# Kernel tuning notes

Measured on AMD Instinct MI355X. Metric: run time of the kernel, lower is better.

## Reference

```python
import jax, jax.numpy as jnp
import numpy as np

V, C, S, H, B, T = 10000, 1024, 128, 256, 16, 128
NEG = -1e10


def _mlp(x, w1, b1, w2, b2, wo, bo):
    # ResidualLayer (dropout=0, eval): relu(lin1) -> relu(lin2 + residual), then final Linear
    h = jax.nn.relu(x @ w1 + b1)
    h = jax.nn.relu(h @ w2 + b2 + x)
    return h @ wo + bo


def setup_inputs() -> dict:
    key = jax.random.key(0)
    ks = iter(jax.random.split(key, 32))
    d = {}
    d["text"] = jax.random.randint(next(ks), (B, T), 0, V)
    d["word2state"] = jax.random.randint(next(ks), (V, S), 0, C)

    def rn(shape, scale):
        return jax.random.normal(next(ks), shape, dtype=jnp.float32) * scale

    s = 1.0 / np.sqrt(H)
    d["start_emb"] = rn((C, H), 1.0)
    d["start_w1"], d["start_b1"] = rn((H, H), s), jnp.zeros((H,), jnp.float32)
    d["start_w2"], d["start_b2"] = rn((H, H), s), jnp.zeros((H,), jnp.float32)
    d["start_wo"], d["start_bo"] = rn((H, 1), s), jnp.zeros((1,), jnp.float32)
    d["state_emb"] = rn((C, H), 1.0)
    d["trans_w1"], d["trans_b1"] = rn((H, H), s), jnp.zeros((H,), jnp.float32)
    d["trans_w2"], d["trans_b2"] = rn((H, H), s), jnp.zeros((H,), jnp.float32)
    d["trans_wo"], d["trans_bo"] = rn((H, C), s), jnp.zeros((C,), jnp.float32)
    d["pre_emb"] = rn((C, H), 1.0)
    d["term_w1"], d["term_b1"] = rn((H, H), s), jnp.zeros((H,), jnp.float32)
    d["term_w2"], d["term_b2"] = rn((H, H), s), jnp.zeros((H,), jnp.float32)
    d["term_wo"], d["term_bo"] = rn((H, V), s), jnp.zeros((V,), jnp.float32)
    return d


def _evidence(text, word2state,
              start_emb, start_w1, start_b1, start_w2, start_b2, start_wo, start_bo,
              state_emb, trans_w1, trans_b1, trans_w2, trans_b2, trans_wo, trans_bo,
              pre_emb, term_w1, term_b1, term_w2, term_b2, term_wo, term_bo):
    # start distribution over C states
    start = jax.nn.log_softmax(
        _mlp(start_emb, start_w1, start_b1, start_w2, start_b2, start_wo, start_bo)[:, 0])
    # transition [C, C]
    transition = jax.nn.log_softmax(
        _mlp(state_emb, trans_w1, trans_b1, trans_w2, trans_b2, trans_wo, trans_bo), axis=-1)
    # emission with sparse state->word mask (scatter of word2state)
    em_logits = _mlp(pre_emb, term_w1, term_b1, term_w2, term_b2, term_wo, term_bo)  # [C, V]
    a = jnp.repeat(jnp.arange(V), S)  # word index per (word, slot)
    mask = jnp.zeros((C, V), dtype=bool).at[word2state.reshape(-1), a].set(True)
    emission = jax.nn.log_softmax(jnp.where(mask, em_logits, NEG), axis=-1)  # [C, V]

    clamped = word2state[text]  # [B, T, S] states allowed per token
    init = start[clamped[:, 0]]  # [B, S]
    # transition restricted to clamped states: [B, T-1, S_prev, S_next]
    lp = transition[clamped[:, :-1, :, None], clamped[:, 1:, None, :]]
    obs = emission[clamped, text[:, :, None]]  # [B, T, S]
    lp = lp + obs[:, 1:, None, :]                     # emission of next token
    lp = lp.at[:, 0].add(init[:, :, None] + obs[:, 0, :, None])
    lp = jnp.swapaxes(lp, -1, -2)  # [B, T-1, S_next, S_prev]

    # forward algorithm (log-space scan)
    alpha = jax.nn.logsumexp(lp[:, 0], axis=-1)  # [B, S]
    pots = jnp.swapaxes(lp[:, 1:], 0, 1)  # [T-2, B, S, S]

    def step(a_prev, pot):
        return jax.nn.logsumexp(pot + a_prev[:, None, :], axis=-1), None

    alpha_T, _ = jax.lax.scan(step, alpha, pots)
    return jax.nn.logsumexp(alpha_T, axis=-1).sum()


def reference(text, word2state,
              start_emb, start_w1, start_b1, start_w2, start_b2, start_wo, start_bo,
              state_emb, trans_w1, trans_b1, trans_w2, trans_b2, trans_wo, trans_bo,
              pre_emb, term_w1, term_b1, term_w2, term_b2, term_wo, term_bo):
    return _evidence(text, word2state,
                     start_emb, start_w1, start_b1, start_w2, start_b2, start_wo, start_bo,
                     state_emb, trans_w1, trans_b1, trans_w2, trans_b2, trans_wo, trans_bo,
                     pre_emb, term_w1, term_b1, term_w2, term_b2, term_wo, term_bo)
```

## Files before the change

### kernel.cpp

```cpp
#include <hip/hip_runtime.h>
#include <hip/hip_bf16.h>

#define V 10000
#define VP 10112
#define C 1024
#define S 128
#define H 256
#define B 16
#define T 128
#define NR 64
#define CHUNK 158
#define NRP 158
#define LDK 40
#define SPITCH 1032

#define TIX(r,g) (((r)<<7) + ((((g) ^ ((r)&7)))<<3))

typedef unsigned short u16;
typedef unsigned int u32;
typedef __bf16 bf16x8 __attribute__((ext_vector_type(8)));
typedef float f32x4 __attribute__((ext_vector_type(4)));

static __device__ __forceinline__ float bf2f(u16 x){ return __uint_as_float(((u32)x)<<16); }
static __device__ __forceinline__ u16 f2bf(float f){ u32 u=__float_as_uint(f); return (u16)((u + 0x7FFFu + ((u>>16)&1u))>>16); }

struct Cvt3 { const float* s0; const float* s1; const float* s2; u16* d0; u16* d1; u16* d2; };
__global__ __launch_bounds__(256) void k_cvt3(Cvt3 a){
  const float* s = (blockIdx.y==0)? a.s0 : (blockIdx.y==1)? a.s1 : a.s2;
  u16* d = (blockIdx.y==0)? a.d0 : (blockIdx.y==1)? a.d1 : a.d2;
  int i = (blockIdx.x*256 + threadIdx.x)*8;
  float4 x0 = *(const float4*)(s+i);
  float4 x1 = *(const float4*)(s+i+4);
  u16 h[8] = {f2bf(x0.x),f2bf(x0.y),f2bf(x0.z),f2bf(x0.w),f2bf(x1.x),f2bf(x1.y),f2bf(x1.z),f2bf(x1.w)};
  *(uint4*)(d+i) = *(uint4*)h;
}

__global__ __launch_bounds__(256) void k_transpose(const float* __restrict__ src, u16* __restrict__ dst, int N){
  __shared__ float tile[32][33];
  int v0 = blockIdx.x*32, k0 = blockIdx.y*32;
  int tx = threadIdx.x, ty = threadIdx.y;
  for (int i=0;i<32;i+=8){
    int k = k0+ty+i, v = v0+tx;
    tile[ty+i][tx] = (v < N) ? src[(size_t)k*N + v] : 0.f;
  }
  __syncthreads();
  for (int i=0;i<32;i+=8){
    int v = v0+ty+i, k = k0+tx;
    dst[(size_t)v*H + k] = f2bf(tile[tx][ty+i]);
  }
}

struct T6 { const float* s[6]; u16* d[6]; };
__global__ __launch_bounds__(256) void k_transpose6(T6 a){
  const float* src = a.s[blockIdx.z];
  u16* dst = a.d[blockIdx.z];
  __shared__ float tile[32][33];
  int v0 = blockIdx.x*32, k0 = blockIdx.y*32;
  int tx = threadIdx.x, ty = threadIdx.y;
  for (int i=0;i<32;i+=8){
    int k = k0+ty+i, v = v0+tx;
    tile[ty+i][tx] = src[(size_t)k*H + v];
  }
  __syncthreads();
  for (int i=0;i<32;i+=8){
    int v = v0+ty+i, k = k0+tx;
    dst[(size_t)v*H + k] = f2bf(tile[tx][ty+i]);
  }
}

struct M3 { const u16* A[3]; const u16* W[3]; const float* bias[3]; const u16* R[3]; u16* O[3]; };
template<int RESID>
__global__ __launch_bounds__(256) void k_mlpg(M3 a){
  const int z = blockIdx.z;
  const u16* A  = a.A[z];
  const u16* BT = a.W[z];
  const float* bias = a.bias[z];
  const u16* Rm = a.R[z];
  u16* O = a.O[z];
  __shared__ u16 As[128*LDK];
  __shared__ u16 Bs[128*LDK];
  const int tid = threadIdx.x;
  const int lane = tid & 63, wave = tid >> 6;
  const int wm = wave >> 1, wn = wave & 1;
  const int m0 = blockIdx.y * 128, n0 = blockIdx.x * 128;
  const int lr = lane & 15, lg = lane >> 4;
  f32x4 acc[4][4] = {};
  const int sr = tid >> 1, sh = (tid & 1) * 16;
  for (int ks = 0; ks < H; ks += 32){
    const u16* ga = A  + (size_t)(m0 + sr)*H + ks + sh;
    const u16* gb = BT + (size_t)(n0 + sr)*H + ks + sh;
    uint4 a0 = *(const uint4*)ga;
    uint4 a1 = *(const uint4*)(ga + 8);
    uint4 b0 = *(const uint4*)gb;
    uint4 b1 = *(const uint4*)(gb + 8);
    __syncthreads();
    *(uint4*)&As[sr*LDK + sh]     = a0;
    *(uint4*)&As[sr*LDK + sh + 8] = a1;
    *(uint4*)&Bs[sr*LDK + sh]     = b0;
    *(uint4*)&Bs[sr*LDK + sh + 8] = b1;
    __syncthreads();
    bf16x8 af[4], bfr[4];
    #pragma unroll
    for (int m=0;m<4;m++) af[m]  = *(const bf16x8*)&As[(wm*64 + m*16 + lr)*LDK + lg*8];
    #pragma unroll
    for (int n=0;n<4;n++) bfr[n] = *(const bf16x8*)&Bs[(wn*64 + n*16 + lr)*LDK + lg*8];
    #pragma unroll
    for (int m=0;m<4;m++)
      #pragma unroll
      for (int n=0;n<4;n++)
        acc[m][n] = __builtin_amdgcn_mfma_f32_16x16x32_bf16(af[m], bfr[n], acc[m][n], 0,0,0);
  }
  #pragma unroll
  for (int m=0;m<4;m++){
    int r_g = m0 + wm*64 + m*16 + lg*4;
    #pragma unroll
    for (int n=0;n<4;n++){
      int n_g = n0 + wn*64 + n*16 + lr;
      float bv = bias[n_g];
      #pragma unroll
      for (int reg=0; reg<4; reg++){
        int r = r_g + reg;
        float val = acc[m][n][reg] + bv;
        if (RESID) val += bf2f(Rm[(size_t)r*H + n_g]);
        val = fmaxf(val, 0.f);
        O[(size_t)r*H + n_g] = f2bf(val);
      }
    }
  }
}

__global__ __launch_bounds__(1024) void k_start(
    const u16* __restrict__ h2, const float* __restrict__ wo, const float* __restrict__ bo,
    float* __restrict__ start_lp){
  const int c = threadIdx.x;
  const int lane = c & 63, wid = c >> 6;
  __shared__ float red[16];
  __shared__ float Ms, Zs;
  float acc = bo[0];
  const u16* row = h2 + (size_t)c*H;
  for (int k=0;k<H;k+=8){
    uint4 hv = *(const uint4*)(row+k);
    float4 w0 = *(const float4*)(wo+k);
    float4 w1 = *(const float4*)(wo+k+4);
    acc = fmaf(bf2f((u16)(hv.x&0xFFFFu)), w0.x, acc);
    acc = fmaf(bf2f((u16)(hv.x>>16)),     w0.y, acc);
    acc = fmaf(bf2f((u16)(hv.y&0xFFFFu)), w0.z, acc);
    acc = fmaf(bf2f((u16)(hv.y>>16)),     w0.w, acc);
    acc = fmaf(bf2f((u16)(hv.z&0xFFFFu)), w1.x, acc);
    acc = fmaf(bf2f((u16)(hv.z>>16)),     w1.y, acc);
    acc = fmaf(bf2f((u16)(hv.w&0xFFFFu)), w1.z, acc);
    acc = fmaf(bf2f((u16)(hv.w>>16)),     w1.w, acc);
  }
  float m = acc;
  for (int o=1;o<64;o<<=1) m = fmaxf(m, __shfl_xor(m,o));
  if (lane==0) red[wid]=m;
  __syncthreads();
  if (c==0){ float t=red[0]; for(int i=1;i<16;i++) t=fmaxf(t,red[i]); Ms=t; }
  __syncthreads();
  float M = Ms;
  float e = expf(acc - M);
  float sum = e;
  for (int o=1;o<64;o<<=1) sum += __shfl_xor(sum,o);
  __syncthreads();
  if (lane==0) red[wid]=sum;
  __syncthreads();
  if (c==0){ float t=0.f; for(int i=0;i<16;i++) t+=red[i]; Zs=t; }
  __syncthreads();
  start_lp[c] = acc - (M + logf(Zs));
}

template<int BIAS_ROW, int BF16OUT, int COLMAX>
__global__ __launch_bounds__(256) void k_gemm(
    const u16* __restrict__ A, const u16* __restrict__ BT,
    const float* __restrict__ bias, int biasBound,
    void* __restrict__ outp, int ldout, float* __restrict__ cmax){
  __shared__ u16 As[128*LDK];
  __shared__ u16 Bs[128*LDK];
  const int tid = threadIdx.x;
  const int lane = tid & 63, wave = tid >> 6;
  const int wm = wave >> 1, wn = wave & 1;
  const int m0 = blockIdx.y * 128, n0 = blockIdx.x * 128;
  const int lr = lane & 15, lg = lane >> 4;
  f32x4 acc[4][4] = {};
  const int sr = tid >> 1, sh = (tid & 1) * 16;
  for (int ks = 0; ks < H; ks += 32){
    const u16* ga = A  + (size_t)(m0 + sr)*H + ks + sh;
    const u16* gb = BT + (size_t)(n0 + sr)*H + ks + sh;
    uint4 a0 = *(const uint4*)ga;
    uint4 a1 = *(const uint4*)(ga + 8);
    uint4 b0 = *(const uint4*)gb;
    uint4 b1 = *(const uint4*)(gb + 8);
    __syncthreads();
    *(uint4*)&As[sr*LDK + sh]     = a0;
    *(uint4*)&As[sr*LDK + sh + 8] = a1;
    *(uint4*)&Bs[sr*LDK + sh]     = b0;
    *(uint4*)&Bs[sr*LDK + sh + 8] = b1;
    __syncthreads();
    bf16x8 af[4], bfr[4];
    #pragma unroll
    for (int m=0;m<4;m++) af[m]  = *(const bf16x8*)&As[(wm*64 + m*16 + lr)*LDK + lg*8];
    #pragma unroll
    for (int n=0;n<4;n++) bfr[n] = *(const bf16x8*)&Bs[(wn*64 + n*16 + lr)*LDK + lg*8];
    #pragma unroll
    for (int m=0;m<4;m++)
      #pragma unroll
      for (int n=0;n<4;n++)
        acc[m][n] = __builtin_amdgcn_mfma_f32_16x16x32_bf16(af[m], bfr[n], acc[m][n], 0,0,0);
  }
  float cmx[4] = {-1e30f,-1e30f,-1e30f,-1e30f};
  #pragma unroll
  for (int m=0;m<4;m++){
    int r_g = m0 + wm*64 + m*16 + lg*4;
    #pragma unroll
    for (int n=0;n<4;n++){
      int n_g = n0 + wn*64 + n*16 + lr;
      float bcol = BIAS_ROW ? 0.f : bias[n_g];
      #pragma unroll
      for (int reg=0; reg<4; reg++){
        int r = r_g + reg;
        float bv = BIAS_ROW ? ((r < biasBound) ? bias[r] : 0.f) : bcol;
        float val = acc[m][n][reg] + bv;
        if (COLMAX) cmx[n] = fmaxf(cmx[n], val);
        if (BF16OUT) ((u16*)outp)[(size_t)r*ldout + n_g] = f2bf(val);
        else         ((float*)outp)[(size_t)r*ldout + n_g] = val;
      }
    }
  }
  if (COLMAX){
    #pragma unroll
    for (int n=0;n<4;n++){
      float m_ = cmx[n];
      m_ = fmaxf(m_, __shfl_xor(m_,16));
      m_ = fmaxf(m_, __shfl_xor(m_,32));
      if (lg==0) cmax[((size_t)(blockIdx.y*2 + wm))*C + n0 + wn*64 + n*16 + lr] = m_;
    }
  }
}

__global__ __launch_bounds__(256) void k_softmax(const float* __restrict__ TL, u16* __restrict__ P){
  const int c = blockIdx.x;
  const int tid = threadIdx.x, lane = tid & 63, wid = tid >> 6;
  __shared__ float red[4];
  __shared__ float Ms, Zs;
  float4 v = ((const float4*)(TL + (size_t)c*C))[tid];
  float m = fmaxf(fmaxf(v.x,v.y), fmaxf(v.z,v.w));
  for (int o=1;o<64;o<<=1) m = fmaxf(m, __shfl_xor(m,o));
  if (lane==0) red[wid] = m;
  __syncthreads();
  if (tid==0) Ms = fmaxf(fmaxf(red[0],red[1]), fmaxf(red[2],red[3]));
  __syncthreads();
  float M = Ms;
  float e0 = expf(v.x-M), e1 = expf(v.y-M), e2 = expf(v.z-M), e3 = expf(v.w-M);
  float s = (e0+e1)+(e2+e3);
  for (int o=1;o<64;o<<=1) s += __shfl_xor(s,o);
  if (lane==0) red[wid] = s;
  __syncthreads();
  if (tid==0) Zs = red[0]+red[1]+red[2]+red[3];
  __syncthreads();
  float inv = 1.f/Zs;
  u32 lo = (u32)f2bf(e0*inv) | ((u32)f2bf(e1*inv)<<16);
  u32 hi = (u32)f2bf(e2*inv) | ((u32)f2bf(e3*inv)<<16);
  *(uint2*)(P + (size_t)c*C + tid*4) = make_uint2(lo, hi);
}

__global__ void k_shiftc(const float* __restrict__ shiftp, float* __restrict__ shift){
  int c = threadIdx.x + blockIdx.x*blockDim.x;
  if (c < C){
    float m = -1e30f;
    for (int r=0;r<NRP;r++) m = fmaxf(m, shiftp[(size_t)r*C + c]);
    shift[c] = m;
  }
}

__global__ __launch_bounds__(256) void k_scatter(
    const int* __restrict__ w2s, const u16* __restrict__ EM,
    const float* __restrict__ shift, u16* __restrict__ D){
  int idx = blockIdx.x*256 + threadIdx.x;
  int v = idx >> 7;
  const int c = w2s[idx];
  float val = bf2f(EM[(size_t)v*C + c]);
  D[(size_t)v*C + c] = f2bf(expf(val - shift[c]));
}

__global__ __launch_bounds__(256) void k_colsum(const u16* __restrict__ D, float* __restrict__ sumexp){
  const int c = blockIdx.x*256 + threadIdx.x;
  const int v0 = blockIdx.y*CHUNK;
  float s = 0.f;
  const u16* p = D + (size_t)v0*C + c;
  #pragma unroll 2
  for (int i=0;i<CHUNK;i++){ s += bf2f(p[0]); p += C; }
  sumexp[(size_t)blockIdx.y*C + c] = s;
}

__global__ void k_lse(const float* __restrict__ shift, const float* __restrict__ sumexp, float* __restrict__ lse){
  int c = threadIdx.x + blockIdx.x*blockDim.x;
  if (c < C){
    float s = 0.f;
    for (int r=0;r<NR;r++) s += sumexp[(size_t)r*C + c];
    lse[c] = shift[c] + logf(s);
  }
}

__global__ __launch_bounds__(128) void k_obs(
    const int* __restrict__ text, const int* __restrict__ w2s,
    const u16* __restrict__ EM, const float* __restrict__ lse,
    float* __restrict__ obs){
  const int bt = blockIdx.x;
  const int s = threadIdx.x;
  const int v = text[bt];
  const int c = w2s[(size_t)v*S + s];
  obs[(size_t)bt*S + s] = bf2f(EM[(size_t)v*C + c]) - lse[c];
}

__global__ __launch_bounds__(256) void k_pair0(
    const int* __restrict__ text, const int* __restrict__ w2s,
    const float* __restrict__ start_lp, const float* __restrict__ obs,
    const u16* __restrict__ P, u16* __restrict__ out, float* __restrict__ scales){
  const int j = blockIdx.x;
  const int b = blockIdx.y;
  const int t0 = 2*j, t1 = 2*j+1;
  __shared__ __align__(16) u16 tile[128*128];
  __shared__ __align__(16) u16 stage[8*SPITCH];
  __shared__ int cp0[S], cp1[S], cn1[S];
  __shared__ float eo0[S], eo1[S], a00[S];
  __shared__ float red[4];
  const int tid = threadIdx.x;
  if (tid < 128){
    int s = tid;
    int cpv = w2s[(size_t)text[b*T + t0]*S + s];
    cp0[s] = cpv;
    cp1[s] = w2s[(size_t)text[b*T + t0+1]*S + s];
    eo0[s] = expf(obs[((size_t)b*T + t0 + 1)*S + s]);
    a00[s] = (t0==0) ? expf(start_lp[cpv] + obs[(size_t)(b*T)*S + s]) : 1.0f;
  } else if (t1 < 127){
    int s = tid-128;
    cn1[s] = w2s[(size_t)text[b*T + t1+1]*S + s];
    eo1[s] = expf(obs[((size_t)b*T + t1 + 1)*S + s]);
  }
  __syncthreads();
  const int lane = tid & 63, wave = tid >> 6;
  const int wm = wave >> 1, wn = wave & 1;
  const int lr = lane & 15, lg = lane >> 4;
  for (int c8 = 0; c8 < 16; ++c8){
    #pragma unroll
    for (int p=0;p<4;p++){
      int idx = p*256 + tid;
      int r = idx >> 7, col16 = idx & 127;
      *(uint4*)&stage[r*SPITCH + col16*8] = *(const uint4*)&P[(size_t)cp0[c8*8 + r]*C + col16*8];
    }
    __syncthreads();
    {
      int r = tid >> 5, kh = tid & 31;
      float asp = a00[c8*8 + r];
      u16 h4[4];
      #pragma unroll
      for (int q=0;q<4;q++){
        int k = kh*4 + q;
        h4[q] = f2bf(bf2f(stage[r*SPITCH + cp1[k]]) * eo0[k] * asp);
      }
      *(uint2*)&tile[TIX(c8*8 + r, kh>>1) + (kh&1)*4] = *(uint2*)h4;
    }
    __syncthreads();
  }
  bf16x8 bfr[4][4];
  #pragma unroll
  for (int n=0;n<4;n++)
    #pragma unroll
    for (int kc=0;kc<4;kc++)
      bfr[n][kc] = *(const bf16x8*)&tile[TIX(wn*64+n*16+lr, kc*4+lg)];
  __syncthreads();
  if (t1 < 127){
    const int sn = tid & 127, half = tid >> 7;
    const int cnv = cn1[sn];
    const float e = eo1[sn];
    for (int c8 = 0; c8 < 16; ++c8){
      #pragma unroll
      for (int p=0;p<4;p++){
        int idx = p*256 + tid;
        int r = idx >> 7, col16 = idx & 127;
        *(uint4*)&stage[r*SPITCH + col16*8] = *(const uint4*)&P[(size_t)cp1[c8*8 + r]*C + col16*8];
      }
      __syncthreads();
      {
        u16 h4[4];
        #pragma unroll
        for (int q=0;q<4;q++){
          int rr = half*4 + q;
          h4[q] = f2bf(bf2f(stage[rr*SPITCH + cnv]) * e);
        }
        *(uint2*)&tile[TIX(sn, c8) + half*4] = *(uint2*)h4;
      }
      __syncthreads();
    }
  } else {
    if (tid < 128){
      int sn = tid;
      #pragma unroll
      for (int g=0; g<16; ++g){
        u16 h8[8];
        #pragma unroll
        for (int q=0;q<8;q++) h8[q] = (g*8+q == sn) ? (u16)0x3F80u : (u16)0u;
        *(uint4*)&tile[TIX(sn, g)] = *(uint4*)h8;
      }
    }
    __syncthreads();
  }
  f32x4 acc[4][4] = {};
  #pragma unroll
  for (int kc=0; kc<4; ++kc){
    bf16x8 af[4];
    #pragma unroll
    for (int m=0;m<4;m++) af[m] = *(const bf16x8*)&tile[TIX(wm*64+m*16+lr, kc*4+lg)];
    #pragma unroll
    for (int m=0;m<4;m++)
      #pragma unroll
      for (int n=0;n<4;n++)
        acc[m][n] = __builtin_amdgcn_mfma_f32_16x16x32_bf16(af[m], bfr[n][kc], acc[m][n], 0,0,0);
  }
  float mx = 0.f;
  #pragma unroll
  for (int m=0;m<4;m++)
    #pragma unroll
    for (int n=0;n<4;n++)
      #pragma unroll
      for (int r=0;r<4;r++) mx = fmaxf(mx, acc[m][n][r]);
  for (int o=1;o<64;o<<=1) mx = fmaxf(mx, __shfl_xor(mx,o));
  if (lane==0) red[wave] = mx;
  __syncthreads();
  mx = fmaxf(fmaxf(red[0],red[1]), fmaxf(red[2],red[3]));
  const float sc = 1.0f / mx;
  if (tid==0) scales[(size_t)b*127 + j] = logf(mx);
  u16* Cg = out + ((size_t)b*64 + j)*(S*S);
  if (j & 1){
    #pragma unroll
    for (int m=0;m<4;m++){
      int rg = wm*64 + m*16 + lg*4;
      #pragma unroll
      for (int n=0;n<4;n++){
        int cg = wn*64 + n*16 + lr;
        #pragma unroll
        for (int r=0;r<4;r++) Cg[(size_t)(rg+r)*128 + cg] = f2bf(acc[m][n][r]*sc);
      }
    }
  } else {
    #pragma unroll
    for (int m=0;m<4;m++){
      int rg = wm*64 + m*16 + lg*4;
      #pragma unroll
      for (int n=0;n<4;n++){
        int cg = wn*64 + n*16 + lr;
        float v0=acc[m][n][0]*sc, v1=acc[m][n][1]*sc, v2=acc[m][n][2]*sc, v3=acc[m][n][3]*sc;
        u32 p0, p1;
        asm("v_cvt_pk_bf16_f32 %0, %1, %2" : "=v"(p0) : "v"(v0), "v"(v1));
        asm("v_cvt_pk_bf16_f32 %0, %1, %2" : "=v"(p1) : "v"(v2), "v"(v3));
        *(uint2*)(Cg + (size_t)cg*128 + rg) = make_uint2(p0, p1);
      }
    }
  }
}

__global__ __launch_bounds__(256) void k_quad(
    const u16* __restrict__ in, u16* __restrict__ out,
    float* __restrict__ scales, int nin, int soff_i, int soff_o){
  const int q = blockIdx.x;
  const int b = blockIdx.y;
  const int nout = nin >> 2;
  const u16* T0 = in + ((size_t)b*nin + 4*q+0)*(S*S);
  const u16* T1 = in + ((size_t)b*nin + 4*q+1)*(S*S);
  const u16* T2 = in + ((size_t)b*nin + 4*q+2)*(S*S);
  const u16* T3 = in + ((size_t)b*nin + 4*q+3)*(S*S);
  __shared__ __align__(16) u16 ldsA[128*128];
  __shared__ __align__(16) u16 ldsB[128*128];
  __shared__ float red[4];
  const int tid = threadIdx.x;
  const int lane = tid & 63, wave = tid >> 6;
  const int wm = wave >> 1, wn = wave & 1;
  const int lr = lane & 15, lg = lane >> 4;
  f32x4 acc[4][4];
  #pragma unroll
  for (int m=0;m<4;m++)
    #pragma unroll
    for (int n=0;n<4;n++) acc[m][n] = (f32x4){0.f,0.f,0.f,0.f};
  #pragma unroll
  for (int kc=0; kc<4; ++kc){
    bf16x8 af[4], bf[4];
    #pragma unroll
    for (int m=0;m<4;m++) af[m] = *(const bf16x8*)(T1 + (size_t)(wm*64+m*16+lr)*128 + kc*32 + lg*8);
    #pragma unroll
    for (int n=0;n<4;n++) bf[n] = *(const bf16x8*)(T0 + (size_t)(wn*64+n*16+lr)*128 + kc*32 + lg*8);
    #pragma unroll
    for (int m=0;m<4;m++)
      #pragma unroll
      for (int n=0;n<4;n++)
        acc[m][n] = __builtin_amdgcn_mfma_f32_16x16x32_bf16(af[m], bf[n], acc[m][n], 0,0,0);
  }
  {
    float mx = 0.f;
    #pragma unroll
    for (int m=0;m<4;m++)
      #pragma unroll
      for (int n=0;n<4;n++)
        #pragma unroll
        for (int r=0;r<4;r++) mx = fmaxf(mx, acc[m][n][r]);
    for (int o=1;o<64;o<<=1) mx = fmaxf(mx, __shfl_xor(mx,o));
    if (lane==0) red[wave] = mx;
    __syncthreads();
    mx = fmaxf(fmaxf(red[0],red[1]), fmaxf(red[2],red[3]));
    float sc = 1.0f/mx;
    if (tid==0) scales[(size_t)b*127 + soff_i + 2*q] = logf(mx);
    #pragma unroll
    for (int m=0;m<4;m++){
      int rg = wm*64 + m*16 + lg*4;
      #pragma unroll
      for (int n=0;n<4;n++){
        int cg = wn*64 + n*16 + lr;
        float v0=acc[m][n][0]*sc, v1=acc[m][n][1]*sc, v2=acc[m][n][2]*sc, v3=acc[m][n][3]*sc;
        u32 p0, p1;
        asm("v_cvt_pk_bf16_f32 %0, %1, %2" : "=v"(p0) : "v"(v0), "v"(v1));
        asm("v_cvt_pk_bf16_f32 %0, %1, %2" : "=v"(p1) : "v"(v2), "v"(v3));
        *(uint2*)&ldsB[TIX(cg, rg>>3) + (rg&7)] = make_uint2(p0, p1);
      }
    }
  }
  __syncthreads();
  #pragma unroll
  for (int m=0;m<4;m++)
    #pragma unroll
    for (int n=0;n<4;n++) acc[m][n] = (f32x4){0.f,0.f,0.f,0.f};
  #pragma unroll
  for (int kc=0; kc<4; ++kc){
    bf16x8 af[4], bf[4];
    #pragma unroll
    for (int m=0;m<4;m++) af[m] = *(const bf16x8*)(T2 + (size_t)(wm*64+m*16+lr)*128 + kc*32 + lg*8);
    #pragma unroll
    for (int n=0;n<4;n++) bf[n] = *(const bf16x8*)(T3 + (size_t)(wn*64+n*16+lr)*128 + kc*32 + lg*8);
    #pragma unroll
    for (int m=0;m<4;m++)
      #pragma unroll
      for (int n=0;n<4;n++)
        acc[m][n] = __builtin_amdgcn_mfma_f32_16x16x32_bf16(af[m], bf[n], acc[m][n], 0,0,0);
  }
  {
    float mx = 0.f;
    #pragma unroll
    for (int m=0;m<4;m++)
      #pragma unroll
      for (int n=0;n<4;n++)
        #pragma unroll
        for (int r=0;r<4;r++) mx = fmaxf(mx, acc[m][n][r]);
    for (int o=1;o<64;o<<=1) mx = fmaxf(mx, __shfl_xor(mx,o));
    __syncthreads();
    if (lane==0) red[wave] = mx;
    __syncthreads();
    mx = fmaxf(fmaxf(red[0],red[1]), fmaxf(red[2],red[3]));
    float sc = 1.0f/mx;
    if (tid==0) scales[(size_t)b*127 + soff_i + 2*q + 1] = logf(mx);
    #pragma unroll
    for (int m=0;m<4;m++){
      int rg = wm*64 + m*16 + lg*4;
      #pragma unroll
      for (int n=0;n<4;n++){
        int cg = wn*64 + n*16 + lr;
        float v0=acc[m][n][0]*sc, v1=acc[m][n][1]*sc, v2=acc[m][n][2]*sc, v3=acc[m][n][3]*sc;
        u32 p0, p1;
        asm("v_cvt_pk_bf16_f32 %0, %1, %2" : "=v"(p0) : "v"(v0), "v"(v1));
        asm("v_cvt_pk_bf16_f32 %0, %1, %2" : "=v"(p1) : "v"(v2), "v"(v3));
        *(uint2*)&ldsA[TIX(cg, rg>>3) + (rg&7)] = make_uint2(p0, p1);
      }
    }
  }
  __syncthreads();
  #pragma unroll
  for (int m=0;m<4;m++)
    #pragma unroll
    for (int n=0;n<4;n++) acc[m][n] = (f32x4){0.f,0.f,0.f,0.f};
  #pragma unroll
  for (int kc=0; kc<4; ++kc){
    bf16x8 af[4], bf[4];
    #pragma unroll
    for (int m=0;m<4;m++) af[m] = *(const bf16x8*)&ldsA[TIX(wm*64+m*16+lr, kc*4+lg)];
    #pragma unroll
    for (int n=0;n<4;n++) bf[n] = *(const bf16x8*)&ldsB[TIX(wn*64+n*16+lr, kc*4+lg)];
    #pragma unroll
    for (int m=0;m<4;m++)
      #pragma unroll
      for (int n=0;n<4;n++)
        acc[m][n] = __builtin_amdgcn_mfma_f32_16x16x32_bf16(af[m], bf[n], acc[m][n], 0,0,0);
  }
  float mx = 0.f;
  #pragma unroll
  for (int m=0;m<4;m++)
    #pragma unroll
    for (int n=0;n<4;n++)
      #pragma unroll
      for (int r=0;r<4;r++) mx = fmaxf(mx, acc[m][n][r]);
  for (int o=1;o<64;o<<=1) mx = fmaxf(mx, __shfl_xor(mx,o));
  __syncthreads();
  if (lane==0) red[wave] = mx;
  __syncthreads();
  mx = fmaxf(fmaxf(red[0],red[1]), fmaxf(red[2],red[3]));
  const float sc = 1.0f / mx;
  if (tid==0) scales[(size_t)b*127 + soff_o + q] = logf(mx);
  u16* Cg = out + ((size_t)b*nout + q)*(S*S);
  if (q & 1){
    #pragma unroll
    for (int m=0;m<4;m++){
      int rg = wm*64 + m*16 + lg*4;
      #pragma unroll
      for (int n=0;n<4;n++){
        int cg = wn*64 + n*16 + lr;
        #pragma unroll
        for (int r=0;r<4;r++) Cg[(size_t)(rg+r)*128 + cg] = f2bf(acc[m][n][r]*sc);
      }
    }
  } else {
    #pragma unroll
    for (int m=0;m<4;m++){
      int rg = wm*64 + m*16 + lg*4;
      #pragma unroll
      for (int n=0;n<4;n++){
        int cg = wn*64 + n*16 + lr;
        float v0=acc[m][n][0]*sc, v1=acc[m][n][1]*sc, v2=acc[m][n][2]*sc, v3=acc[m][n][3]*sc;
        u32 p0, p1;
        asm("v_cvt_pk_bf16_f32 %0, %1, %2" : "=v"(p0) : "v"(v0), "v"(v1));
        asm("v_cvt_pk_bf16_f32 %0, %1, %2" : "=v"(p1) : "v"(v2), "v"(v3));
        *(uint2*)(Cg + (size_t)cg*128 + rg) = make_uint2(p0, p1);
      }
    }
  }
}

__global__ __launch_bounds__(256) void k_fin4(
    const u16* __restrict__ in, const float* __restrict__ scales, float* __restrict__ res){
  const int b = blockIdx.x;
  const u16* T0 = in + ((size_t)b*4 + 0)*(S*S);
  const u16* T1 = in + ((size_t)b*4 + 1)*(S*S);
  const u16* T2 = in + ((size_t)b*4 + 2)*(S*S);
  const u16* T3 = in + ((size_t)b*4 + 3)*(S*S);
  __shared__ __align__(16) u16 ldsA[128*128];
  __shared__ __align__(16) u16 ldsB[128*128];
  __shared__ float red[8];
  __shared__ float sloc[2];
  const int tid = threadIdx.x;
  const int lane = tid & 63, wave = tid >> 6;
  const int wm = wave >> 1, wn = wave & 1;
  const int lr = lane & 15, lg = lane >> 4;
  f32x4 acc[4][4];
  #pragma unroll
  for (int m=0;m<4;m++)
    #pragma unroll
    for (int n=0;n<4;n++) acc[m][n] = (f32x4){0.f,0.f,0.f,0.f};
  #pragma unroll
  for (int kc=0; kc<4; ++kc){
    bf16x8 af[4], bf[4];
    #pragma unroll
    for (int m=0;m<4;m++) af[m] = *(const bf16x8*)(T1 + (size_t)(wm*64+m*16+lr)*128 + kc*32 + lg*8);
    #pragma unroll
    for (int n=0;n<4;n++) bf[n] = *(const bf16x8*)(T0 + (size_t)(wn*64+n*16+lr)*128 + kc*32 + lg*8);
    #pragma unroll
    for (int m=0;m<4;m++)
      #pragma unroll
      for (int n=0;n<4;n++)
        acc[m][n] = __builtin_amdgcn_mfma_f32_16x16x32_bf16(af[m], bf[n], acc[m][n], 0,0,0);
  }
  {
    float mx = 0.f;
    #pragma unroll
    for (int m=0;m<4;m++)
      #pragma unroll
      for (int n=0;n<4;n++)
        #pragma unroll
        for (int r=0;r<4;r++) mx = fmaxf(mx, acc[m][n][r]);
    for (int o=1;o<64;o<<=1) mx = fmaxf(mx, __shfl_xor(mx,o));
    if (lane==0) red[wave] = mx;
    __syncthreads();
    mx = fmaxf(fmaxf(red[0],red[1]), fmaxf(red[2],red[3]));
    float sc = 1.0f/mx;
    if (tid==0) sloc[0] = logf(mx);
    #pragma unroll
    for (int m=0;m<4;m++){
      int rg = wm*64 + m*16 + lg*4;
      #pragma unroll
      for (int n=0;n<4;n++){
        int cg = wn*64 + n*16 + lr;
        float v0=acc[m][n][0]*sc, v1=acc[m][n][1]*sc, v2=acc[m][n][2]*sc, v3=acc[m][n][3]*sc;
        u32 p0, p1;
        asm("v_cvt_pk_bf16_f32 %0, %1, %2" : "=v"(p0) : "v"(v0), "v"(v1));
        asm("v_cvt_pk_bf16_f32 %0, %1, %2" : "=v"(p1) : "v"(v2), "v"(v3));
        *(uint2*)&ldsB[TIX(cg, rg>>3) + (rg&7)] = make_uint2(p0, p1);
      }
    }
  }
  __syncthreads();
  #pragma unroll
  for (int m=0;m<4;m++)
    #pragma unroll
    for (int n=0;n<4;n++) acc[m][n] = (f32x4){0.f,0.f,0.f,0.f};
  #pragma unroll
  for (int kc=0; kc<4; ++kc){
    bf16x8 af[4], bf[4];
    #pragma unroll
    for (int m=0;m<4;m++) af[m] = *(const bf16x8*)(T2 + (size_t)(wm*64+m*16+lr)*128 + kc*32 + lg*8);
    #pragma unroll
    for (int n=0;n<4;n++) bf[n] = *(const bf16x8*)(T3 + (size_t)(wn*64+n*16+lr)*128 + kc*32 + lg*8);
    #pragma unroll
    for (int m=0;m<4;m++)
      #pragma unroll
      for (int n=0;n<4;n++)
        acc[m][n] = __builtin_amdgcn_mfma_f32_16x16x32_bf16(af[m], bf[n], acc[m][n], 0,0,0);
  }
  {
    float mx = 0.f;
    #pragma unroll
    for (int m=0;m<4;m++)
      #pragma unroll
      for (int n=0;n<4;n++)
        #pragma unroll
        for (int r=0;r<4;r++) mx = fmaxf(mx, acc[m][n][r]);
    for (int o=1;o<64;o<<=1) mx = fmaxf(mx, __shfl_xor(mx,o));
    __syncthreads();
    if (lane==0) red[wave] = mx;
    __syncthreads();
    mx = fmaxf(fmaxf(red[0],red[1]), fmaxf(red[2],red[3]));
    float sc = 1.0f/mx;
    if (tid==0) sloc[1] = logf(mx);
    #pragma unroll
    for (int m=0;m<4;m++){
      int rg = wm*64 + m*16 + lg*4;
      #pragma unroll
      for (int n=0;n<4;n++){
        int cg = wn*64 + n*16 + lr;
        float v0=acc[m][n][0]*sc, v1=acc[m][n][1]*sc, v2=acc[m][n][2]*sc, v3=acc[m][n][3]*sc;
        u32 p0, p1;
        asm("v_cvt_pk_bf16_f32 %0, %1, %2" : "=v"(p0) : "v"(v0), "v"(v1));
        asm("v_cvt_pk_bf16_f32 %0, %1, %2" : "=v"(p1) : "v"(v2), "v"(v3));
        *(uint2*)&ldsA[TIX(cg, rg>>3) + (rg&7)] = make_uint2(p0, p1);
      }
    }
  }
  __syncthreads();
  #pragma unroll
  for (int m=0;m<4;m++)
    #pragma unroll
    for (int n=0;n<4;n++) acc[m][n] = (f32x4){0.f,0.f,0.f,0.f};
  #pragma unroll
  for (int kc=0; kc<4; ++kc){
    bf16x8 af[4], bf[4];
    #pragma unroll
    for (int m=0;m<4;m++) af[m] = *(const bf16x8*)&ldsA[TIX(wm*64+m*16+lr, kc*4+lg)];
    #pragma unroll
    for (int n=0;n<4;n++) bf[n] = *(const bf16x8*)&ldsB[TIX(wn*64+n*16+lr, kc*4+lg)];
    #pragma unroll
    for (int m=0;m<4;m++)
      #pragma unroll
      for (int n=0;n<4;n++)
        acc[m][n] = __builtin_amdgcn_mfma_f32_16x16x32_bf16(af[m], bf[n], acc[m][n], 0,0,0);
  }
  float s = 0.f;
  #pragma unroll
  for (int m=0;m<4;m++)
    #pragma unroll
    for (int n=0;n<4;n++)
      #pragma unroll
      for (int r=0;r<4;r++) s += acc[m][n][r];
  for (int o=1;o<64;o<<=1) s += __shfl_xor(s,o);
  float sl = (tid < 124) ? scales[(size_t)b*127 + tid] : 0.f;
  for (int o=1;o<64;o<<=1) sl += __shfl_xor(sl,o);
  __syncthreads();
  if (lane==0){ red[wave] = s; red[4+wave] = sl; }
  __syncthreads();
  if (tid==0){
    float tot  = red[0]+red[1]+red[2]+red[3];
    float ssum = red[4]+red[5]+red[6]+red[7];
    res[b] = logf(tot) + ssum + sloc[0] + sloc[1];
  }
}

__global__ void k_final(const float* __restrict__ res, float* __restrict__ out){
  if (threadIdx.x==0){
    float s = 0.f;
    for (int i=0;i<B;i++) s += res[i];
    out[0] = s;
  }
}

extern "C" void kernel_launch(void* const* d_in, const int* in_sizes, int n_in,
                              void* d_out, int out_size, void* d_ws, size_t ws_size,
                              hipStream_t stream){
  const int*   text      = (const int*)d_in[0];
  const int*   w2s       = (const int*)d_in[1];
  const float* start_emb = (const float*)d_in[2];
  const float* start_w1  = (const float*)d_in[3];
  const float* start_b1  = (const float*)d_in[4];
  const float* start_w2  = (const float*)d_in[5];
  const float* start_b2  = (const float*)d_in[6];
  const float* start_wo  = (const float*)d_in[7];
  const float* start_bo  = (const float*)d_in[8];
  const float* state_emb = (const float*)d_in[9];
  const float* trans_w1  = (const float*)d_in[10];
  const float* trans_b1  = (const float*)d_in[11];
  const float* trans_w2  = (const float*)d_in[12];
  const float* trans_b2  = (const float*)d_in[13];
  const float* trans_wo  = (const float*)d_in[14];
  const float* trans_bo  = (const float*)d_in[15];
  const float* pre_emb   = (const float*)d_in[16];
  const float* term_w1   = (const float*)d_in[17];
  const float* term_b1   = (const float*)d_in[18];
  const float* term_w2   = (const float*)d_in[19];
  const float* term_b2   = (const float*)d_in[20];
  const float* term_wo   = (const float*)d_in[21];
  const float* term_bo   = (const float*)d_in[22];

  char* ws = (char*)d_ws;
  size_t off = 0;
  auto alloc = [&](size_t bytes)->char*{ char* p = ws + off; off += (bytes + 255) & ~(size_t)255; return p; };
  u16*   embb     = (u16*)  alloc(sizeof(u16)*3*(size_t)C*H);
  u16*   h1b      = (u16*)  alloc(sizeof(u16)*3*(size_t)C*H);
  u16*   h2b      = (u16*)  alloc(sizeof(u16)*3*(size_t)C*H);
  u16*   wt       = (u16*)  alloc(sizeof(u16)*6*(size_t)H*H);
  float* start_lp = (float*)alloc(sizeof(float)*C);
  float* shift    = (float*)alloc(sizeof(float)*C);
  float* shiftp   = (float*)alloc(sizeof(float)*(size_t)C*NRP);
  float* sumexp   = (float*)alloc(sizeof(float)*(size_t)C*NR);
  float* lse      = (float*)alloc(sizeof(float)*C);
  float* resb     = (float*)alloc(sizeof(float)*B);
  float* scales   = (float*)alloc(sizeof(float)*(size_t)B*127);
  u16*   P        = (u16*)  alloc(sizeof(u16)*(size_t)C*C);
  u16*   wotb     = (u16*)  alloc(sizeof(u16)*(size_t)VP*H);
  u16*   wottr    = (u16*)  alloc(sizeof(u16)*(size_t)C*H);
  float* obs      = (float*)alloc(sizeof(float)*(size_t)B*T*S);
  u16*   EM       = (u16*)  alloc(sizeof(u16)*(size_t)VP*C);
  u16*   treeA    = (u16*)  alloc(sizeof(u16)*(size_t)B*64*S*S);
  u16*   treeB    = (u16*)  alloc(sizeof(u16)*(size_t)B*16*S*S);
  float* TL       = (float*)treeA;
  u16*   D        = (u16*)((char*)treeA + sizeof(float)*(size_t)C*C);
  (void)ws_size; (void)in_sizes; (void)n_in; (void)out_size;

  u16* embb0 = embb, *embb1 = embb + (size_t)C*H, *embb2 = embb + 2*(size_t)C*H;
  u16* h1b0 = h1b, *h1b1 = h1b + (size_t)C*H, *h1b2 = h1b + 2*(size_t)C*H;
  u16* h2b0 = h2b, *h2b1 = h2b + (size_t)C*H, *h2b2 = h2b + 2*(size_t)C*H;

  hipMemsetAsync(D, 0, sizeof(u16)*(size_t)VP*C, stream);

  Cvt3 cv; cv.s0 = start_emb; cv.s1 = state_emb; cv.s2 = pre_emb;
  cv.d0 = embb0; cv.d1 = embb1; cv.d2 = embb2;
  k_cvt3<<<dim3(C*H/(256*8), 3), dim3(256), 0, stream>>>(cv);

  T6 t6;
  t6.s[0]=start_w1; t6.s[1]=start_w2; t6.s[2]=trans_w1; t6.s[3]=trans_w2; t6.s[4]=term_w1; t6.s[5]=term_w2;
  for (int i=0;i<6;i++) t6.d[i] = wt + (size_t)i*H*H;
  k_transpose6<<<dim3(H/32, H/32, 6), dim3(32,8), 0, stream>>>(t6);

  M3 l1;
  l1.A[0]=embb0; l1.A[1]=embb1; l1.A[2]=embb2;
  l1.W[0]=wt;    l1.W[1]=wt+2*(size_t)H*H; l1.W[2]=wt+4*(size_t)H*H;
  l1.bias[0]=start_b1; l1.bias[1]=trans_b1; l1.bias[2]=term_b1;
  l1.R[0]=l1.R[1]=l1.R[2]=nullptr;
  l1.O[0]=h1b0; l1.O[1]=h1b1; l1.O[2]=h1b2;
  k_mlpg<0><<<dim3(H/128, C/128, 3), dim3(256), 0, stream>>>(l1);

  M3 l2;
  l2.A[0]=h1b0; l2.A[1]=h1b1; l2.A[2]=h1b2;
  l2.W[0]=wt+(size_t)H*H; l2.W[1]=wt+3*(size_t)H*H; l2.W[2]=wt+5*(size_t)H*H;
  l2.bias[0]=start_b2; l2.bias[1]=trans_b2; l2.bias[2]=term_b2;
  l2.R[0]=embb0; l2.R[1]=embb1; l2.R[2]=embb2;
  l2.O[0]=h2b0; l2.O[1]=h2b1; l2.O[2]=h2b2;
  k_mlpg<1><<<dim3(H/128, C/128, 3), dim3(256), 0, stream>>>(l2);

  k_start<<<dim3(1), dim3(1024), 0, stream>>>(h2b0, start_wo, start_bo, start_lp);
  k_transpose<<<dim3(VP/32, H/32), dim3(32,8), 0, stream>>>(term_wo, wotb, V);
  k_transpose<<<dim3(C/32, H/32), dim3(32,8), 0, stream>>>(trans_wo, wottr, C);
  k_gemm<0,0,0><<<dim3(C/128, C/128), dim3(256), 0, stream>>>(h2b1, wottr, trans_bo, C, TL, C, nullptr);
  k_softmax<<<dim3(C), dim3(256), 0, stream>>>(TL, P);
  k_gemm<1,1,1><<<dim3(C/128, VP/128), dim3(256), 0, stream>>>(wotb, h2b2, term_bo, V, EM, C, shiftp);
  k_shiftc<<<dim3((C+255)/256), dim3(256), 0, stream>>>(shiftp, shift);
  k_scatter<<<dim3(V*S/256), dim3(256), 0, stream>>>(w2s, EM, shift, D);
  k_colsum<<<dim3(C/256, NR), dim3(256), 0, stream>>>(D, sumexp);
  k_lse<<<dim3((C+255)/256), dim3(256), 0, stream>>>(shift, sumexp, lse);
  k_obs<<<dim3(B*T), dim3(128), 0, stream>>>(text, w2s, EM, lse, obs);

  k_pair0<<<dim3(64, B), dim3(256), 0, stream>>>(text, w2s, start_lp, obs, P, treeA, scales);
  k_quad<<<dim3(16, B), dim3(256), 0, stream>>>(treeA, treeB, scales, 64, 64, 96);
  k_quad<<<dim3(4,  B), dim3(256), 0, stream>>>(treeB, treeA, scales, 16, 112, 120);
  k_fin4<<<dim3(B), dim3(256), 0, stream>>>(treeA, scales, resb);
  k_final<<<dim3(1), dim3(64), 0, stream>>>(resb, (float*)d_out);
}
```

Baseline: 277.4 us.

## Fuse prep kernels, replace dense scatter/colsum with bitmask sumexp, inline obs

Merges the bf16 conversion and all weight transposes into a single prep launch. Replaces the memset, dense scatter matrix and column-sum pass with a per-block shared-memory kernel that deduplicates (word,state) pairs with a bitmask and accumulates exp values atomically. Removes the obs kernel by computing emissions directly inside pair0, and rewrites pair0's gather to read P elements directly instead of staging whole rows through LDS. This saves launches and a large memset/write/read of the 20MB dense buffer, at the cost of LDS atomics and uncoalesced scalar P gathers.

```diff
diff --git a/kernel.cpp b/kernel.cpp
--- a/kernel.cpp
+++ b/kernel.cpp
@@ -8,11 +8,10 @@
 #define H 256
 #define B 16
 #define T 128
-#define NR 64
-#define CHUNK 158
 #define NRP 158
+#define NSB 157
 #define LDK 40
-#define SPITCH 1032
+#define PITCH 136
 
 #define TIX(r,g) (((r)<<7) + ((((g) ^ ((r)&7)))<<3))
 
@@ -24,42 +23,45 @@
 static __device__ __forceinline__ float bf2f(u16 x){ return __uint_as_float(((u32)x)<<16); }
 static __device__ __forceinline__ u16 f2bf(float f){ u32 u=__float_as_uint(f); return (u16)((u + 0x7FFFu + ((u>>16)&1u))>>16); }
 
-struct Cvt3 { const float* s0; const float* s1; const float* s2; u16* d0; u16* d1; u16* d2; };
-__global__ __launch_bounds__(256) void k_cvt3(Cvt3 a){
-  const float* s = (blockIdx.y==0)? a.s0 : (blockIdx.y==1)? a.s1 : a.s2;
-  u16* d = (blockIdx.y==0)? a.d0 : (blockIdx.y==1)? a.d1 : a.d2;
-  int i = (blockIdx.x*256 + threadIdx.x)*8;
-  float4 x0 = *(const float4*)(s+i);
-  float4 x1 = *(const float4*)(s+i+4);
-  u16 h[8] = {f2bf(x0.x),f2bf(x0.y),f2bf(x0.z),f2bf(x0.w),f2bf(x1.x),f2bf(x1.y),f2bf(x1.z),f2bf(x1.w)};
-  *(uint4*)(d+i) = *(uint4*)h;
-}
-
-__global__ __launch_bounds__(256) void k_transpose(const float* __restrict__ src, u16* __restrict__ dst, int N){
+struct Prep {
+  const float* cs[3]; u16* cd[3];
+  const float* ts[6]; u16* td[6];
+  const float* wvs; u16* wvd;
+  const float* wcs; u16* wcd;
+};
+__global__ __launch_bounds__(256) void k_prep(Prep a){
+  const int blk = blockIdx.x;
+  const int tid = threadIdx.x;
+  if (blk < 384){
+    int z = blk >> 7, bx = blk & 127;
+    const float* s = a.cs[z]; u16* d = a.cd[z];
+    int i = (bx*256 + tid)*8;
+    float4 x0 = *(const float4*)(s+i);
+    float4 x1 = *(const float4*)(s+i+4);
+    u16 h[8] = {f2bf(x0.x),f2bf(x0.y),f2bf(x0.z),f2bf(x0.w),f2bf(x1.x),f2bf(x1.y),f2bf(x1.z),f2bf(x1.w)};
+    *(uint4*)(d+i) = *(uint4*)h;
+    return;
+  }
   __shared__ float tile[32][33];
-  int v0 = blockIdx.x*32, k0 = blockIdx.y*32;
-  int tx = threadIdx.x, ty = threadIdx.y;
+  const int tx = tid & 31, ty = tid >> 5;
+  const float* src; u16* dst; int N, ldsrc, v0, k0;
+  if (blk < 768){
+    int sub = blk - 384;
+    int z = sub >> 6, rem = sub & 63;
+    src = a.ts[z]; dst = a.td[z]; N = H; ldsrc = H;
+    v0 = (rem & 7)*32; k0 = (rem >> 3)*32;
+  } else if (blk < 3296){
+    int sub = blk - 768;
+    src = a.wvs; dst = a.wvd; N = V; ldsrc = V;
+    v0 = (sub % 316)*32; k0 = (sub / 316)*32;
+  } else {
+    int sub = blk - 3296;
+    src = a.wcs; dst = a.wcd; N = C; ldsrc = C;
+    v0 = (sub & 31)*32; k0 = (sub >> 5)*32;
+  }
   for (int i=0;i<32;i+=8){
     int k = k0+ty+i, v = v0+tx;
-    tile[ty+i][tx] = (v < N) ? src[(size_t)k*N + v] : 0.f;
-  }
-  __syncthreads();
-  for (int i=0;i<32;i+=8){
-    int v = v0+ty+i, k = k0+tx;
-    dst[(size_t)v*H + k] = f2bf(tile[tx][ty+i]);
-  }
-}
-
-struct T6 { const float* s[6]; u16* d[6]; };
-__global__ __launch_bounds__(256) void k_transpose6(T6 a){
-  const float* src = a.s[blockIdx.z];
-  u16* dst = a.d[blockIdx.z];
-  __shared__ float tile[32][33];
-  int v0 = blockIdx.x*32, k0 = blockIdx.y*32;
-  int tx = threadIdx.x, ty = threadIdx.y;
-  for (int i=0;i<32;i+=8){
-    int k = k0+ty+i, v = v0+tx;
-    tile[ty+i][tx] = src[(size_t)k*H + v];
+    tile[ty+i][tx] = (v < N) ? src[(size_t)k*ldsrc + v] : 0.f;
   }
   __syncthreads();
   for (int i=0;i<32;i+=8){
@@ -272,145 +274,128 @@
   }
 }
 
-__global__ __launch_bounds__(256) void k_scatter(
+__global__ __launch_bounds__(256) void k_sumexp(
     const int* __restrict__ w2s, const u16* __restrict__ EM,
-    const float* __restrict__ shift, u16* __restrict__ D){
-  int idx = blockIdx.x*256 + threadIdx.x;
-  int v = idx >> 7;
-  const int c = w2s[idx];
-  float val = bf2f(EM[(size_t)v*C + c]);
-  D[(size_t)v*C + c] = f2bf(expf(val - shift[c]));
-}
-
-__global__ __launch_bounds__(256) void k_colsum(const u16* __restrict__ D, float* __restrict__ sumexp){
-  const int c = blockIdx.x*256 + threadIdx.x;
-  const int v0 = blockIdx.y*CHUNK;
-  float s = 0.f;
-  const u16* p = D + (size_t)v0*C + c;
+    const float* __restrict__ shift, float* __restrict__ sumexp){
+  __shared__ float accL[C];
+  __shared__ u32 bm[64*32];
+  const int tid = threadIdx.x;
+  const int v0 = blockIdx.x*64;
+  #pragma unroll
+  for (int i=0;i<4;i++) accL[tid + i*256] = 0.f;
+  #pragma unroll
+  for (int i=0;i<8;i++) bm[tid + i*256] = 0u;
+  __syncthreads();
   #pragma unroll 2
-  for (int i=0;i<CHUNK;i++){ s += bf2f(p[0]); p += C; }
-  sumexp[(size_t)blockIdx.y*C + c] = s;
+  for (int it=0; it<32; ++it){
+    int e = it*256 + tid;
+    int vl = e >> 7, s = e & 127;
+    int v = v0 + vl;
+    if (v < V){
+      int c = w2s[(size_t)v*S + s];
+      u32 old = atomicOr(&bm[(vl<<5) + (c>>5)], 1u << (c&31));
+      if (!((old >> (c&31)) & 1u))
+        atomicAdd(&accL[c], expf(bf2f(EM[(size_t)v*C + c]) - shift[c]));
+    }
+  }
+  __syncthreads();
+  float* dst = sumexp + (size_t)blockIdx.x*C;
+  #pragma unroll
+  for (int i=0;i<4;i++) dst[tid + i*256] = accL[tid + i*256];
 }
 
 __global__ void k_lse(const float* __restrict__ shift, const float* __restrict__ sumexp, float* __restrict__ lse){
   int c = threadIdx.x + blockIdx.x*blockDim.x;
   if (c < C){
     float s = 0.f;
-    for (int r=0;r<NR;r++) s += sumexp[(size_t)r*C + c];
+    for (int r=0;r<NSB;r++) s += sumexp[(size_t)r*C + c];
     lse[c] = shift[c] + logf(s);
   }
-}
-
-__global__ __launch_bounds__(128) void k_obs(
-    const int* __restrict__ text, const int* __restrict__ w2s,
-    const u16* __restrict__ EM, const float* __restrict__ lse,
-    float* __restrict__ obs){
-  const int bt = blockIdx.x;
-  const int s = threadIdx.x;
-  const int v = text[bt];
-  const int c = w2s[(size_t)v*S + s];
-  obs[(size_t)bt*S + s] = bf2f(EM[(size_t)v*C + c]) - lse[c];
 }
 
 __global__ __launch_bounds__(256) void k_pair0(
     const int* __restrict__ text, const int* __restrict__ w2s,
-    const float* __restrict__ start_lp, const float* __restrict__ obs,
-    const u16* __restrict__ P, u16* __restrict__ out, float* __restrict__ scales){
+    const float* __restrict__ start_lp, const float* __restrict__ lse,
+    const u16* __restrict__ EM, const u16* __restrict__ P,
+    u16* __restrict__ out, float* __restrict__ scales){
   const int j = blockIdx.x;
   const int b = blockIdx.y;
   const int t0 = 2*j, t1 = 2*j+1;
-  __shared__ __align__(16) u16 tile[128*128];
-  __shared__ __align__(16) u16 stage[8*SPITCH];
-  __shared__ int cp0[S], cp1[S], cn1[S];
+  __shared__ __align__(16) u16 tile[128*PITCH];
+  __shared__ int cp0[S], cs1[S], cn1[S];
   __shared__ float eo0[S], eo1[S], a00[S];
   __shared__ float red[4];
   const int tid = threadIdx.x;
   if (tid < 128){
     int s = tid;
-    int cpv = w2s[(size_t)text[b*T + t0]*S + s];
-    cp0[s] = cpv;
-    cp1[s] = w2s[(size_t)text[b*T + t0+1]*S + s];
-    eo0[s] = expf(obs[((size_t)b*T + t0 + 1)*S + s]);
-    a00[s] = (t0==0) ? expf(start_lp[cpv] + obs[(size_t)(b*T)*S + s]) : 1.0f;
+    int v0 = text[b*T + t0], v1 = text[b*T + t0 + 1];
+    int c0 = w2s[(size_t)v0*S + s];
+    int c1 = w2s[(size_t)v1*S + s];
+    cp0[s] = c0;
+    cs1[s] = c1;
+    eo0[s] = expf(bf2f(EM[(size_t)v1*C + c1]) - lse[c1]);
+    a00[s] = (t0==0) ? expf(start_lp[c0] + bf2f(EM[(size_t)v0*C + c0]) - lse[c0]) : 1.0f;
   } else if (t1 < 127){
     int s = tid-128;
-    cn1[s] = w2s[(size_t)text[b*T + t1+1]*S + s];
-    eo1[s] = expf(obs[((size_t)b*T + t1 + 1)*S + s]);
-  }
-  __syncthreads();
+    int v2 = text[b*T + t1 + 1];
+    int c2 = w2s[(size_t)v2*S + s];
+    cn1[s] = c2;
+    eo1[s] = expf(bf2f(EM[(size_t)v2*C + c2]) - lse[c2]);
+  }
+  __syncthreads();
+  const int sn = tid & 127, half = tid >> 7;
   const int lane = tid & 63, wave = tid >> 6;
   const int wm = wave >> 1, wn = wave & 1;
   const int lr = lane & 15, lg = lane >> 4;
-  for (int c8 = 0; c8 < 16; ++c8){
-    #pragma unroll
-    for (int p=0;p<4;p++){
-      int idx = p*256 + tid;
-      int r = idx >> 7, col16 = idx & 127;
-      *(uint4*)&stage[r*SPITCH + col16*8] = *(const uint4*)&P[(size_t)cp0[c8*8 + r]*C + col16*8];
-    }
-    __syncthreads();
-    {
-      int r = tid >> 5, kh = tid & 31;
-      float asp = a00[c8*8 + r];
-      u16 h4[4];
-      #pragma unroll
-      for (int q=0;q<4;q++){
-        int k = kh*4 + q;
-        h4[q] = f2bf(bf2f(stage[r*SPITCH + cp1[k]]) * eo0[k] * asp);
-      }
-      *(uint2*)&tile[TIX(c8*8 + r, kh>>1) + (kh&1)*4] = *(uint2*)h4;
-    }
-    __syncthreads();
-  }
+  {
+    const float e = eo0[sn];
+    const int cnv = cs1[sn];
+    for (int it=0; it<64; ++it){
+      int sp = it*2 + half;
+      float v = bf2f(P[(size_t)cp0[sp]*C + cnv]) * e * a00[sp];
+      tile[sp*PITCH + sn] = f2bf(v);
+    }
+  }
+  __syncthreads();
   bf16x8 bfr[4][4];
   #pragma unroll
   for (int n=0;n<4;n++)
     #pragma unroll
     for (int kc=0;kc<4;kc++)
-      bfr[n][kc] = *(const bf16x8*)&tile[TIX(wn*64+n*16+lr, kc*4+lg)];
+      bfr[n][kc] = *(const bf16x8*)&tile[(wn*64+n*16+lr)*PITCH + kc*32 + lg*8];
   __syncthreads();
   if (t1 < 127){
-    const int sn = tid & 127, half = tid >> 7;
+    const float e = eo1[sn];
     const int cnv = cn1[sn];
-    const float e = eo1[sn];
-    for (int c8 = 0; c8 < 16; ++c8){
-      #pragma unroll
-      for (int p=0;p<4;p++){
-        int idx = p*256 + tid;
-        int r = idx >> 7, col16 = idx & 127;
-        *(uint4*)&stage[r*SPITCH + col16*8] = *(const uint4*)&P[(size_t)cp1[c8*8 + r]*C + col16*8];
-      }
-      __syncthreads();
-      {
-        u16 h4[4];
-        #pragma unroll
-        for (int q=0;q<4;q++){
-          int rr = half*4 + q;
-          h4[q] = f2bf(bf2f(stage[rr*SPITCH + cnv]) * e);
-        }
-        *(uint2*)&tile[TIX(sn, c8) + half*4] = *(uint2*)h4;
-      }
-      __syncthreads();
+    #pragma unroll
+    for (int g=0; g<8; ++g){
+      u16 h[8];
+      #pragma unroll
+      for (int q=0; q<8; ++q){
+        int sp = half*64 + g*8 + q;
+        h[q] = f2bf(bf2f(P[(size_t)cs1[sp]*C + cnv]) * e);
+      }
+      *(uint4*)&tile[sn*PITCH + half*64 + g*8] = *(uint4*)h;
     }
   } else {
-    if (tid < 128){
-      int sn = tid;
-      #pragma unroll
-      for (int g=0; g<16; ++g){
-        u16 h8[8];
-        #pragma unroll
-        for (int q=0;q<8;q++) h8[q] = (g*8+q == sn) ? (u16)0x3F80u : (u16)0u;
-        *(uint4*)&tile[TIX(sn, g)] = *(uint4*)h8;
-      }
-    }
-    __syncthreads();
-  }
+    #pragma unroll
+    for (int g=0; g<8; ++g){
+      u16 h[8];
+      #pragma unroll
+      for (int q=0; q<8; ++q){
+        int sp = half*64 + g*8 + q;
+        h[q] = (sn == sp) ? (u16)0x3F80u : (u16)0u;
+      }
+      *(uint4*)&tile[sn*PITCH + half*64 + g*8] = *(uint4*)h;
+    }
+  }
+  __syncthreads();
   f32x4 acc[4][4] = {};
   #pragma unroll
   for (int kc=0; kc<4; ++kc){
     bf16x8 af[4];
     #pragma unroll
-    for (int m=0;m<4;m++) af[m] = *(const bf16x8*)&tile[TIX(wm*64+m*16+lr, kc*4+lg)];
+    for (int m=0;m<4;m++) af[m] = *(const bf16x8*)&tile[(wm*64+m*16+lr)*PITCH + kc*32 + lg*8];
     #pragma unroll
     for (int m=0;m<4;m++)
       #pragma unroll
@@ -821,35 +806,31 @@
   float* start_lp = (float*)alloc(sizeof(float)*C);
   float* shift    = (float*)alloc(sizeof(float)*C);
   float* shiftp   = (float*)alloc(sizeof(float)*(size_t)C*NRP);
-  float* sumexp   = (float*)alloc(sizeof(float)*(size_t)C*NR);
+  float* sumexp   = (float*)alloc(sizeof(float)*(size_t)C*NSB);
   float* lse      = (float*)alloc(sizeof(float)*C);
   float* resb     = (float*)alloc(sizeof(float)*B);
   float* scales   = (float*)alloc(sizeof(float)*(size_t)B*127);
   u16*   P        = (u16*)  alloc(sizeof(u16)*(size_t)C*C);
   u16*   wotb     = (u16*)  alloc(sizeof(u16)*(size_t)VP*H);
   u16*   wottr    = (u16*)  alloc(sizeof(u16)*(size_t)C*H);
-  float* obs      = (float*)alloc(sizeof(float)*(size_t)B*T*S);
   u16*   EM       = (u16*)  alloc(sizeof(u16)*(size_t)VP*C);
   u16*   treeA    = (u16*)  alloc(sizeof(u16)*(size_t)B*64*S*S);
   u16*   treeB    = (u16*)  alloc(sizeof(u16)*(size_t)B*16*S*S);
   float* TL       = (float*)treeA;
-  u16*   D        = (u16*)((char*)treeA + sizeof(float)*(size_t)C*C);
   (void)ws_size; (void)in_sizes; (void)n_in; (void)out_size;
 
   u16* embb0 = embb, *embb1 = embb + (size_t)C*H, *embb2 = embb + 2*(size_t)C*H;
   u16* h1b0 = h1b, *h1b1 = h1b + (size_t)C*H, *h1b2 = h1b + 2*(size_t)C*H;
   u16* h2b0 = h2b, *h2b1 = h2b + (size_t)C*H, *h2b2 = h2b + 2*(size_t)C*H;
 
-  hipMemsetAsync(D, 0, sizeof(u16)*(size_t)VP*C, stream);
-
-  Cvt3 cv; cv.s0 = start_emb; cv.s1 = state_emb; cv.s2 = pre_emb;
-  cv.d0 = embb0; cv.d1 = embb1; cv.d2 = embb2;
-  k_cvt3<<<dim3(C*H/(256*8), 3), dim3(256), 0, stream>>>(cv);
-
-  T6 t6;
-  t6.s[0]=start_w1; t6.s[1]=start_w2; t6.s[2]=trans_w1; t6.s[3]=trans_w2; t6.s[4]=term_w1; t6.s[5]=term_w2;
-  for (int i=0;i<6;i++) t6.d[i] = wt + (size_t)i*H*H;
-  k_transpose6<<<dim3(H/32, H/32, 6), dim3(32,8), 0, stream>>>(t6);
+  Prep pr;
+  pr.cs[0]=start_emb; pr.cs[1]=state_emb; pr.cs[2]=pre_emb;
+  pr.cd[0]=embb0; pr.cd[1]=embb1; pr.cd[2]=embb2;
+  pr.ts[0]=start_w1; pr.ts[1]=start_w2; pr.ts[2]=trans_w1; pr.ts[3]=trans_w2; pr.ts[4]=term_w1; pr.ts[5]=term_w2;
+  for (int i=0;i<6;i++) pr.td[i] = wt + (size_t)i*H*H;
+  pr.wvs = term_wo; pr.wvd = wotb;
+  pr.wcs = trans_wo; pr.wcd = wottr;
+  k_prep<<<dim3(3552), dim3(256), 0, stream>>>(pr);
 
   M3 l1;
   l1.A[0]=embb0; l1.A[1]=embb1; l1.A[2]=embb2;
@@ -868,18 +849,14 @@
   k_mlpg<1><<<dim3(H/128, C/128, 3), dim3(256), 0, stream>>>(l2);
 
   k_start<<<dim3(1), dim3(1024), 0, stream>>>(h2b0, start_wo, start_bo, start_lp);
-  k_transpose<<<dim3(VP/32, H/32), dim3(32,8), 0, stream>>>(term_wo, wotb, V);
-  k_transpose<<<dim3(C/32, H/32), dim3(32,8), 0, stream>>>(trans_wo, wottr, C);
   k_gemm<0,0,0><<<dim3(C/128, C/128), dim3(256), 0, stream>>>(h2b1, wottr, trans_bo, C, TL, C, nullptr);
   k_softmax<<<dim3(C), dim3(256), 0, stream>>>(TL, P);
   k_gemm<1,1,1><<<dim3(C/128, VP/128), dim3(256), 0, stream>>>(wotb, h2b2, term_bo, V, EM, C, shiftp);
   k_shiftc<<<dim3((C+255)/256), dim3(256), 0, stream>>>(shiftp, shift);
-  k_scatter<<<dim3(V*S/256), dim3(256), 0, stream>>>(w2s, EM, shift, D);
-  k_colsum<<<dim3(C/256, NR), dim3(256), 0, stream>>>(D, sumexp);
+  k_sumexp<<<dim3(NSB), dim3(256), 0, stream>>>(w2s, EM, shift, sumexp);
   k_lse<<<dim3((C+255)/256), dim3(256), 0, stream>>>(shift, sumexp, lse);
-  k_obs<<<dim3(B*T), dim3(128), 0, stream>>>(text, w2s, EM, lse, obs);
-
-  k_pair0<<<dim3(64, B), dim3(256), 0, stream>>>(text, w2s, start_lp, obs, P, treeA, scales);
+
+  k_pair0<<<dim3(64, B), dim3(256), 0, stream>>>(text, w2s, start_lp, lse, EM, P, treeA, scales);
   k_quad<<<dim3(16, B), dim3(256), 0, stream>>>(treeA, treeB, scales, 64, 64, 96);
   k_quad<<<dim3(4,  B), dim3(256), 0, stream>>>(treeB, treeA, scales, 16, 112, 120);
   k_fin4<<<dim3(B), dim3(256), 0, stream>>>(treeA, scales, resb);
```

Result: faster. 255.2 us (-8.0%).
